# Optimization experiments

Measured on AMD Instinct MI355X. Metric: run time of the kernel, lower is better.

## Reference

```python
import jax, jax.numpy as jnp
import numpy as np

TEMPERATURE = 0.1
LOSS_SCALE = 1.0
LAMBD = 0.5


def setup_inputs() -> dict:
    key = jax.random.key(0)
    k1, k2 = jax.random.split(key)
    B, D = 4096, 768
    predicted = jax.random.normal(k1, (B, D), dtype=jnp.float32)
    target = jax.random.normal(k2, (B, D), dtype=jnp.float32)
    return {"predicted": predicted, "target": target}


def reference(predicted, target):
    predicted = predicted.astype(jnp.float32)
    target = target.astype(jnp.float32)
    B = predicted.shape[0]

    # Pairwise L2 distances via Gram identity (avoids B x B x D intermediate):
    # ||p_i - t_j||^2 = ||p_i||^2 + ||t_j||^2 - 2 p_i . t_j
    p_sq = jnp.sum(predicted * predicted, axis=-1)  # [B]
    t_sq = jnp.sum(target * target, axis=-1)        # [B]
    cross = predicted @ target.T                    # [B, B]
    sq_dist = p_sq[:, None] + t_sq[None, :] - 2.0 * cross
    distances = jnp.sqrt(jnp.maximum(sq_dist, 0.0))  # [B, B]

    logits = -distances / TEMPERATURE
    # cross-entropy with labels = arange(B): mean of -log_softmax diagonal
    log_probs = jax.nn.log_softmax(logits, axis=-1)
    contrastive_dist_loss = -jnp.mean(jnp.diagonal(log_probs))

    # normalized L1 magnitude loss
    elementwise_l1 = jnp.sum(jnp.abs(predicted - target), axis=-1)  # [B]
    target_magnitude = jnp.sum(jnp.abs(target), axis=-1)            # [B]
    norm_factor = jax.lax.stop_gradient(target_magnitude)
    normalized_magnitude_loss = jnp.mean(elementwise_l1 / norm_factor)

    total_loss = LOSS_SCALE * (
        LAMBD * contrastive_dist_loss + (1.0 - LAMBD) * normalized_magnitude_loss
    )
    return (total_loss, contrastive_dist_loss, normalized_magnitude_loss)
```

## Files before the change

### kernel.cpp

```cpp
#include <hip/hip_runtime.h>
#include <hip/hip_bf16.h>
#include <math.h>

#define B_ROWS 4096
#define D_DIM  768

#define BM 128
#define BN 128
#define BK 64
#define NKT (D_DIM / BK)

typedef __attribute__((ext_vector_type(8))) short bf16x8;
typedef __attribute__((ext_vector_type(4))) float f32x4;

__device__ __forceinline__ unsigned short f32_to_bf16(float x) {
    unsigned int u = __float_as_uint(x);
    return (unsigned short)((u + 0x7fffu + ((u >> 16) & 1u)) >> 16);
}

__device__ __forceinline__ void async_copy16(const unsigned short* g, unsigned short* l) {
    __builtin_amdgcn_global_load_lds(
        (const __attribute__((address_space(1))) unsigned int*)g,
        (__attribute__((address_space(3))) unsigned int*)l,
        16, 0, 0);
}

__global__ void __launch_bounds__(256) rowstats_kernel(
    const float* __restrict__ P, const float* __restrict__ T,
    unsigned short* __restrict__ Pb, unsigned short* __restrict__ Tb,
    float* __restrict__ p_sq, float* __restrict__ t_sq,
    float* __restrict__ diagl, float* __restrict__ magr,
    float* __restrict__ rowsum)
{
    const int wave = threadIdx.x >> 6, lane = threadIdx.x & 63;
    const int i = blockIdx.x * 4 + wave;
    const f32x4* prow = (const f32x4*)(P + (size_t)i * D_DIM);
    const f32x4* trow = (const f32x4*)(T + (size_t)i * D_DIM);
    ushort4* pbrow = (ushort4*)(Pb + (size_t)i * D_DIM);
    ushort4* tbrow = (ushort4*)(Tb + (size_t)i * D_DIM);

    float psq = 0.f, tsq = 0.f, cr = 0.f, l1 = 0.f, tm = 0.f;
    #pragma unroll
    for (int u = 0; u < 3; ++u) {
        const int c4 = u * 64 + lane;
        f32x4 p = prow[c4], t = trow[c4];
        #pragma unroll
        for (int k = 0; k < 4; ++k) {
            psq += p[k] * p[k]; tsq += t[k] * t[k]; cr += p[k] * t[k];
            l1 += fabsf(p[k] - t[k]); tm += fabsf(t[k]);
        }
        pbrow[c4] = make_ushort4(f32_to_bf16(p[0]), f32_to_bf16(p[1]),
                                 f32_to_bf16(p[2]), f32_to_bf16(p[3]));
        tbrow[c4] = make_ushort4(f32_to_bf16(t[0]), f32_to_bf16(t[1]),
                                 f32_to_bf16(t[2]), f32_to_bf16(t[3]));
    }
    #pragma unroll
    for (int m = 1; m < 64; m <<= 1) {
        psq += __shfl_xor(psq, m, 64);
        tsq += __shfl_xor(tsq, m, 64);
        cr  += __shfl_xor(cr,  m, 64);
        l1  += __shfl_xor(l1,  m, 64);
        tm  += __shfl_xor(tm,  m, 64);
    }
    if (lane == 0) {
        p_sq[i] = psq;
        t_sq[i] = tsq;
        float sq = fmaxf(psq + tsq - 2.0f * cr, 0.0f);
        diagl[i] = -sqrtf(sq) * 10.0f;
        magr[i]  = l1 / tm;
        rowsum[i] = 0.0f;
    }
}

__global__ void __launch_bounds__(256) lse_gemm_kernel(
    const unsigned short* __restrict__ Pb, const unsigned short* __restrict__ Tb,
    const float* __restrict__ p_sq, const float* __restrict__ t_sq,
    const float* __restrict__ diagl, float* __restrict__ rowsum)
{
    __shared__ __align__(16) unsigned short As[2][BM * BK];
    __shared__ __align__(16) unsigned short Bs[2][BN * BK];

    const int tid = threadIdx.x;

    const int flat = blockIdx.y * (B_ROWS / BN) + blockIdx.x;
    const int xcd  = flat & 7;
    const int s    = flat >> 3;
    const int g    = xcd + ((s >> 6) << 3);
    const int w    = s & 63;
    const int i0   = (((g >> 2) << 3) + (w >> 3)) * BM;
    const int j0   = (((g & 3) << 3) + (w & 7)) * BN;

    const int lane  = tid & 63;
    const int wave  = tid >> 6;
    const int wm    = wave >> 1, wn = wave & 1;
    const int row16 = lane & 15, quad = lane >> 4;
    const int m_base = wm * 64, n_base = wn * 64;

    const int lrow   = lane >> 3;
    const int lchunk = (lane & 7) ^ lrow;
    const int swz = (quad ^ (row16 & 7)) << 4;

    const unsigned short* pg[4];
    const unsigned short* tg[4];
    #pragma unroll
    for (int it = 0; it < 4; ++it) {
        const int r = wave * 32 + it * 8 + lrow;
        pg[it] = Pb + (size_t)(i0 + r) * D_DIM + lchunk * 8;
        tg[it] = Tb + (size_t)(j0 + r) * D_DIM + lchunk * 8;
    }

    f32x4 acc[4][4];
    #pragma unroll
    for (int a = 0; a < 4; ++a)
        #pragma unroll
        for (int b = 0; b < 4; ++b)
            acc[a][b] = (f32x4){0.f, 0.f, 0.f, 0.f};

    #pragma unroll
    for (int it = 0; it < 4; ++it) {
        async_copy16(pg[it], &As[0][(wave * 4 + it) * 512]);
        async_copy16(tg[it], &Bs[0][(wave * 4 + it) * 512]);
    }

    for (int ktile = 0; ktile < NKT; ++ktile) {
        const int sel = ktile & 1;
        __syncthreads();

        if (ktile + 1 < NKT) {
            const int kt1 = (ktile + 1) * BK;
            #pragma unroll
            for (int it = 0; it < 4; ++it) {
                async_copy16(pg[it] + kt1, &As[sel ^ 1][(wave * 4 + it) * 512]);
                async_copy16(tg[it] + kt1, &Bs[sel ^ 1][(wave * 4 + it) * 512]);
            }
        }

        const char* Ab = (const char*)As[sel];
        const char* Bb = (const char*)Bs[sel];
        #pragma unroll
        for (int ks = 0; ks < BK; ks += 32) {
            const int kx = ks ? 64 : 0;
            bf16x8 a[4], b[4];
            #pragma unroll
            for (int mt = 0; mt < 4; ++mt) {
                const int off = (m_base + mt * 16 + row16) * 128 + swz;
                a[mt] = *(const bf16x8*)(Ab + (off ^ kx));
            }
            #pragma unroll
            for (int nt = 0; nt < 4; ++nt) {
                const int off = (n_base + nt * 16 + row16) * 128 + swz;
                b[nt] = *(const bf16x8*)(Bb + (off ^ kx));
            }
            #pragma unroll
            for (int mt = 0; mt < 4; ++mt)
                #pragma unroll
                for (int nt = 0; nt < 4; ++nt)
                    acc[mt][nt] = __builtin_amdgcn_mfma_f32_16x16x32_bf16(
                        a[mt], b[nt], acc[mt][nt], 0, 0, 0);
        }
    }

    const float NT_LOG2E = -14.4269504089f;
    const float LOG2E    = 1.44269504089f;
    float tsq_l[4];
    #pragma unroll
    for (int nt = 0; nt < 4; ++nt)
        tsq_l[nt] = t_sq[j0 + n_base + nt * 16 + row16];

    #pragma unroll
    for (int mt = 0; mt < 4; ++mt) {
        #pragma unroll
        for (int r = 0; r < 4; ++r) {
            const int i = i0 + m_base + mt * 16 + quad * 4 + r;
            const float psq = p_sq[i];
            const float c0  = -diagl[i] * LOG2E;
            float sfin = 0.f;
            #pragma unroll
            for (int nt = 0; nt < 4; ++nt) {
                float c  = acc[mt][nt][r];
                float sq = fmaxf(fmaf(-2.0f, c, psq + tsq_l[nt]), 0.0f);
                float d  = sqrtf(sq);
                float y  = fmaf(d, NT_LOG2E, c0);
                sfin += exp2f(y);
            }
            #pragma unroll
            for (int m = 1; m < 16; m <<= 1) sfin += __shfl_xor(sfin, m, 64);
            if (row16 == 0) atomicAdd(&rowsum[i], sfin);
        }
    }
}

__global__ void __launch_bounds__(256) finalize_kernel(
    const float* __restrict__ rowsum, const float* __restrict__ magr,
    float* __restrict__ out)
{
    const int tid = threadIdx.x;
    double sc = 0.0, sm = 0.0;
    for (int i = tid; i < B_ROWS; i += 256) {
        sc += log((double)rowsum[i]);
        sm += (double)magr[i];
    }
    #pragma unroll
    for (int m = 1; m < 64; m <<= 1) {
        sc += __shfl_xor(sc, m, 64);
        sm += __shfl_xor(sm, m, 64);
    }
    __shared__ double red[4][2];
    const int wave = tid >> 6, lane = tid & 63;
    if (lane == 0) { red[wave][0] = sc; red[wave][1] = sm; }
    __syncthreads();
    if (tid == 0) {
        sc = red[0][0] + red[1][0] + red[2][0] + red[3][0];
        sm = red[0][1] + red[1][1] + red[2][1] + red[3][1];
        double lc = sc / (double)B_ROWS;
        double lm = sm / (double)B_ROWS;
        out[0] = (float)(0.5 * lc + 0.5 * lm);
        out[1] = (float)lc;
        out[2] = (float)lm;
    }
}

extern "C" void kernel_launch(void* const* d_in, const int* in_sizes, int n_in,
                              void* d_out, int out_size, void* d_ws, size_t ws_size,
                              hipStream_t stream) {
    const float* P = (const float*)d_in[0];
    const float* T = (const float*)d_in[1];
    float* out = (float*)d_out;

    char* ws = (char*)d_ws;
    float* rowsum = (float*)ws;               ws += B_ROWS * sizeof(float);
    float* p_sq   = (float*)ws;               ws += B_ROWS * sizeof(float);
    float* t_sq   = (float*)ws;               ws += B_ROWS * sizeof(float);
    float* diagl  = (float*)ws;               ws += B_ROWS * sizeof(float);
    float* magr   = (float*)ws;               ws += B_ROWS * sizeof(float);
    unsigned short* Pb = (unsigned short*)ws; ws += (size_t)B_ROWS * D_DIM * 2;
    unsigned short* Tb = (unsigned short*)ws;

    rowstats_kernel<<<B_ROWS / 4, 256, 0, stream>>>(
        P, T, Pb, Tb, p_sq, t_sq, diagl, magr, rowsum);
    lse_gemm_kernel<<<dim3(B_ROWS / BN, B_ROWS / BM), 256, 0, stream>>>(
        Pb, Tb, p_sq, t_sq, diagl, rowsum);
    finalize_kernel<<<1, 256, 0, stream>>>(rowsum, magr, out);
}
```

Before: 131.2 us.

## Use register-staged single-buffer loads and fuse finalize via last-block counter

Replaces the async global-to-LDS double-buffered copies with register prefetch of the next K tile into a single LDS buffer. This halves LDS use, which may raise occupancy, but adds an extra barrier per tile. It also removes the separate finalize kernel: the last GEMM block, found through an atomic counter that rowstats resets, does the final log-sum reduction. That saves one launch at the cost of a threadfence and an atomic per block.

Result: slower. 288.5 us (+119.9%).

```diff
diff --git a/kernel.cpp b/kernel.cpp
--- a/kernel.cpp
+++ b/kernel.cpp
@@ -9,6 +9,8 @@
 #define BN 128
 #define BK 64
 #define NKT (D_DIM / BK)
+#define NBLK (B_ROWS / BM)
+#define GRID_TILES (NBLK * NBLK)
 
 typedef __attribute__((ext_vector_type(8))) short bf16x8;
 typedef __attribute__((ext_vector_type(4))) float f32x4;
@@ -16,13 +18,6 @@
 __device__ __forceinline__ unsigned short f32_to_bf16(float x) {
     unsigned int u = __float_as_uint(x);
     return (unsigned short)((u + 0x7fffu + ((u >> 16) & 1u)) >> 16);
-}
-
-__device__ __forceinline__ void async_copy16(const unsigned short* g, unsigned short* l) {
-    __builtin_amdgcn_global_load_lds(
-        (const __attribute__((address_space(1))) unsigned int*)g,
-        (__attribute__((address_space(3))) unsigned int*)l,
-        16, 0, 0);
 }
 
 __global__ void __launch_bounds__(256) rowstats_kernel(
@@ -30,8 +25,9 @@
     unsigned short* __restrict__ Pb, unsigned short* __restrict__ Tb,
     float* __restrict__ p_sq, float* __restrict__ t_sq,
     float* __restrict__ diagl, float* __restrict__ magr,
-    float* __restrict__ rowsum)
+    float* __restrict__ rowsum, unsigned int* __restrict__ counter)
 {
+    if (blockIdx.x == 0 && threadIdx.x == 0) *counter = 0u;
     const int wave = threadIdx.x >> 6, lane = threadIdx.x & 63;
     const int i = blockIdx.x * 4 + wave;
     const f32x4* prow = (const f32x4*)(P + (size_t)i * D_DIM);
@@ -75,14 +71,16 @@
 __global__ void __launch_bounds__(256) lse_gemm_kernel(
     const unsigned short* __restrict__ Pb, const unsigned short* __restrict__ Tb,
     const float* __restrict__ p_sq, const float* __restrict__ t_sq,
-    const float* __restrict__ diagl, float* __restrict__ rowsum)
+    const float* __restrict__ diagl, const float* __restrict__ magr,
+    float* __restrict__ rowsum, unsigned int* __restrict__ counter,
+    float* __restrict__ out)
 {
-    __shared__ __align__(16) unsigned short As[2][BM * BK];
-    __shared__ __align__(16) unsigned short Bs[2][BN * BK];
+    __shared__ __align__(16) unsigned short As[BM * BK];
+    __shared__ __align__(16) unsigned short Bs[BN * BK];
 
     const int tid = threadIdx.x;
 
-    const int flat = blockIdx.y * (B_ROWS / BN) + blockIdx.x;
+    const int flat = blockIdx.y * NBLK + blockIdx.x;
     const int xcd  = flat & 7;
     const int s    = flat >> 3;
     const int g    = xcd + ((s >> 6) << 3);
@@ -95,19 +93,15 @@
     const int wm    = wave >> 1, wn = wave & 1;
     const int row16 = lane & 15, quad = lane >> 4;
     const int m_base = wm * 64, n_base = wn * 64;
-
-    const int lrow   = lane >> 3;
-    const int lchunk = (lane & 7) ^ lrow;
     const int swz = (quad ^ (row16 & 7)) << 4;
 
-    const unsigned short* pg[4];
-    const unsigned short* tg[4];
-    #pragma unroll
-    for (int it = 0; it < 4; ++it) {
-        const int r = wave * 32 + it * 8 + lrow;
-        pg[it] = Pb + (size_t)(i0 + r) * D_DIM + lchunk * 8;
-        tg[it] = Tb + (size_t)(j0 + r) * D_DIM + lchunk * 8;
-    }
+    const int c8 = tid & 7;
+    const int r0 = tid >> 3;
+    const int sw = c8 ^ (r0 & 7);
+    const int4* gpA = (const int4*)Pb + (size_t)(i0 + r0) * (D_DIM / 8) + c8;
+    const int4* gpB = (const int4*)Tb + (size_t)(j0 + r0) * (D_DIM / 8) + c8;
+    int4* lwA = (int4*)&As[r0 * 64 + sw * 8];
+    int4* lwB = (int4*)&Bs[r0 * 64 + sw * 8];
 
     f32x4 acc[4][4];
     #pragma unroll
@@ -116,27 +110,33 @@
         for (int b = 0; b < 4; ++b)
             acc[a][b] = (f32x4){0.f, 0.f, 0.f, 0.f};
 
+    int4 ps[4], tsg[4];
     #pragma unroll
     for (int it = 0; it < 4; ++it) {
-        async_copy16(pg[it], &As[0][(wave * 4 + it) * 512]);
-        async_copy16(tg[it], &Bs[0][(wave * 4 + it) * 512]);
-    }
+        ps[it]  = gpA[it * 3072];
+        tsg[it] = gpB[it * 3072];
+    }
+
+    const char* Ab = (const char*)As;
+    const char* Bb = (const char*)Bs;
 
     for (int ktile = 0; ktile < NKT; ++ktile) {
-        const int sel = ktile & 1;
+        if (ktile) __syncthreads();
+        #pragma unroll
+        for (int it = 0; it < 4; ++it) {
+            lwA[it * 256] = ps[it];
+            lwB[it * 256] = tsg[it];
+        }
+        if (ktile + 1 < NKT) {
+            const int ko = (ktile + 1) * 8;
+            #pragma unroll
+            for (int it = 0; it < 4; ++it) {
+                ps[it]  = gpA[it * 3072 + ko];
+                tsg[it] = gpB[it * 3072 + ko];
+            }
+        }
         __syncthreads();
 
-        if (ktile + 1 < NKT) {
-            const int kt1 = (ktile + 1) * BK;
-            #pragma unroll
-            for (int it = 0; it < 4; ++it) {
-                async_copy16(pg[it] + kt1, &As[sel ^ 1][(wave * 4 + it) * 512]);
-                async_copy16(tg[it] + kt1, &Bs[sel ^ 1][(wave * 4 + it) * 512]);
-            }
-        }
-
-        const char* Ab = (const char*)As[sel];
-        const char* Bb = (const char*)Bs[sel];
         #pragma unroll
         for (int ks = 0; ks < BK; ks += 32) {
             const int kx = ks ? 64 : 0;
@@ -188,35 +188,38 @@
             if (row16 == 0) atomicAdd(&rowsum[i], sfin);
         }
     }
-}
-
-__global__ void __launch_bounds__(256) finalize_kernel(
-    const float* __restrict__ rowsum, const float* __restrict__ magr,
-    float* __restrict__ out)
-{
-    const int tid = threadIdx.x;
-    double sc = 0.0, sm = 0.0;
-    for (int i = tid; i < B_ROWS; i += 256) {
-        sc += log((double)rowsum[i]);
-        sm += (double)magr[i];
-    }
-    #pragma unroll
-    for (int m = 1; m < 64; m <<= 1) {
-        sc += __shfl_xor(sc, m, 64);
-        sm += __shfl_xor(sm, m, 64);
-    }
-    __shared__ double red[4][2];
-    const int wave = tid >> 6, lane = tid & 63;
-    if (lane == 0) { red[wave][0] = sc; red[wave][1] = sm; }
+
+    __threadfence();
+    __shared__ unsigned int lastflag;
+    if (tid == 0) {
+        unsigned int old = atomicAdd(counter, 1u);
+        lastflag = (old == (unsigned)(GRID_TILES - 1)) ? 1u : 0u;
+    }
     __syncthreads();
-    if (tid == 0) {
-        sc = red[0][0] + red[1][0] + red[2][0] + red[3][0];
-        sm = red[0][1] + red[1][1] + red[2][1] + red[3][1];
-        double lc = sc / (double)B_ROWS;
-        double lm = sm / (double)B_ROWS;
-        out[0] = (float)(0.5 * lc + 0.5 * lm);
-        out[1] = (float)lc;
-        out[2] = (float)lm;
+    if (lastflag) {
+        double sc = 0.0, sm = 0.0;
+        for (int i = tid; i < B_ROWS; i += 256) {
+            float rs = atomicAdd(&rowsum[i], 0.0f);
+            sc += log((double)rs);
+            sm += (double)magr[i];
+        }
+        #pragma unroll
+        for (int m = 1; m < 64; m <<= 1) {
+            sc += __shfl_xor(sc, m, 64);
+            sm += __shfl_xor(sm, m, 64);
+        }
+        __shared__ double red[4][2];
+        if ((tid & 63) == 0) { red[tid >> 6][0] = sc; red[tid >> 6][1] = sm; }
+        __syncthreads();
+        if (tid == 0) {
+            sc = red[0][0] + red[1][0] + red[2][0] + red[3][0];
+            sm = red[0][1] + red[1][1] + red[2][1] + red[3][1];
+            double lc = sc / (double)B_ROWS;
+            double lm = sm / (double)B_ROWS;
+            out[0] = (float)(0.5 * lc + 0.5 * lm);
+            out[1] = (float)lc;
+            out[2] = (float)lm;
+        }
     }
 }
 
@@ -233,12 +236,12 @@
     float* t_sq   = (float*)ws;               ws += B_ROWS * sizeof(float);
     float* diagl  = (float*)ws;               ws += B_ROWS * sizeof(float);
     float* magr   = (float*)ws;               ws += B_ROWS * sizeof(float);
+    unsigned int* counter = (unsigned int*)ws; ws += 16;
     unsigned short* Pb = (unsigned short*)ws; ws += (size_t)B_ROWS * D_DIM * 2;
     unsigned short* Tb = (unsigned short*)ws;
 
     rowstats_kernel<<<B_ROWS / 4, 256, 0, stream>>>(
-        P, T, Pb, Tb, p_sq, t_sq, diagl, magr, rowsum);
-    lse_gemm_kernel<<<dim3(B_ROWS / BN, B_ROWS / BM), 256, 0, stream>>>(
-        Pb, Tb, p_sq, t_sq, diagl, rowsum);
-    finalize_kernel<<<1, 256, 0, stream>>>(rowsum, magr, out);
-}
+        P, T, Pb, Tb, p_sq, t_sq, diagl, magr, rowsum, counter);
+    lse_gemm_kernel<<<dim3(NBLK, NBLK), 256, 0, stream>>>(
+        Pb, Tb, p_sq, t_sq, diagl, magr, rowsum, counter, out);
+}
```
